# Performance work log

Measured on AMD Instinct MI355X. Metric: run time of the kernel, lower is better.

The kernel has to match this reference:

```python
import jax, jax.numpy as jnp
import numpy as np

EPS = 1e-5

def setup_inputs() -> dict:
    key = jax.random.key(0)
    ks = jax.random.split(key, 8)
    b, c, p, h = 8, 128, 2048, 4
    inp = {
        "input": jax.random.normal(ks[0], (b, c, p), jnp.float32),
        "gamma": jnp.ones((c,), jnp.float32),
        "beta": jnp.zeros((c,), jnp.float32),
        "Wq": jax.random.normal(ks[1], (c * h, c), jnp.float32) * (c ** -0.5),
        "bq": jnp.zeros((c * h,), jnp.float32),
        "Wk": jax.random.normal(ks[2], (c * h, c), jnp.float32) * (c ** -0.5),
        "bk": jnp.zeros((c * h,), jnp.float32),
        "Wv": jax.random.normal(ks[3], (c * h, c), jnp.float32) * (c ** -0.5),
        "bv": jnp.zeros((c * h,), jnp.float32),
        "Wo": jax.random.normal(ks[4], (c, c * h), jnp.float32) * ((c * h) ** -0.5),
        "bo": jnp.zeros((c,), jnp.float32),
    }
    return inp


def reference(input, gamma, beta, Wq, bq, Wk, bk, Wv, bv, Wo, bo):
    b, c, p = input.shape
    h = Wq.shape[0] // c
    # BatchNorm1d (training-mode batch stats): mean/var per channel over (batch, points)
    mean = jnp.mean(input, axis=(0, 2), keepdims=True)          # [1,c,1]
    var = jnp.mean((input - mean) ** 2, axis=(0, 2), keepdims=True)
    x = (input - mean) * jax.lax.rsqrt(var + EPS)
    x = x * gamma[None, :, None] + beta[None, :, None]
    # 1x1 conv projections == channel matmuls; then split c*h -> (c, h)
    q = (jnp.einsum('oc,bcp->bop', Wq, x) + bq[None, :, None]).reshape(b, c, h, p)
    k = (jnp.einsum('oc,bcp->bop', Wk, x) + bk[None, :, None]).reshape(b, c, h, p)
    v = (jnp.einsum('oc,bcp->bop', Wv, x) + bv[None, :, None]).reshape(b, c, h, p)
    # attention over points; scale by c**-0.5
    weight = jnp.einsum('bchi,bchj->bhij', q, k) * (c ** -0.5)   # [b,h,p,p]
    weight = jax.nn.softmax(weight, axis=3)
    att = jnp.einsum('bhij,bchj->bchi', weight, v)               # [b,c,h,p]
    att = att.reshape(b, c * h, p)
    out = jnp.einsum('oc,bcp->bop', Wo, att) + bo[None, :, None]
    return out + input
```

## Files before the change

### kernel.cpp

```cpp
#include <hip/hip_runtime.h>
#include <hip/hip_bf16.h>

#define NB 8
#define NC 128
#define NP 2048
#define NH 4
#define NCH 512

typedef __attribute__((ext_vector_type(8))) short bf16x8;
typedef __attribute__((ext_vector_type(16))) float f32x16;

__device__ __forceinline__ float bf2f(unsigned short u) {
  return __uint_as_float(((unsigned)u) << 16);
}
__device__ __forceinline__ unsigned short f2bf(float f) {
  __hip_bfloat16 h = __float2bfloat16(f);
  return *reinterpret_cast<unsigned short*>(&h);
}
__device__ __forceinline__ unsigned cvtpk(float lo, float hi) {
  unsigned r;
  asm("v_cvt_pk_bf16_f32 %0, %1, %2" : "=v"(r) : "v"(lo), "v"(hi));
  return r;
}
__device__ __forceinline__ void gload_lds16(const void* g, void* l) {
  __builtin_amdgcn_global_load_lds(
      (const __attribute__((address_space(1))) void*)g,
      (__attribute__((address_space(3))) void*)l, 16, 0, 0);
}
__device__ __forceinline__ void plswap(unsigned& a, unsigned& b) {
  asm volatile("v_permlane32_swap_b32 %0, %1" : "+v"(a), "+v"(b));
}

__global__ __launch_bounds__(256) void bn_partial(
    const float* __restrict__ in, float* __restrict__ psum,
    float* __restrict__ psum2) {
  int c = blockIdx.x >> 2, qtr = blockIdx.x & 3;
  int t = threadIdx.x;
  float s = 0.f, s2 = 0.f;
  for (int b = 0; b < NB; ++b) {
    const float* ptr = in + ((size_t)b * NC + c) * NP + qtr * 512;
    #pragma unroll
    for (int p = 0; p < 2; ++p) {
      float v = ptr[p * 256 + t];
      s += v; s2 += v * v;
    }
  }
  for (int off = 32; off; off >>= 1) {
    s += __shfl_down(s, off, 64);
    s2 += __shfl_down(s2, off, 64);
  }
  __shared__ float red[8];
  int lane = t & 63, wid = t >> 6;
  if (!lane) { red[wid] = s; red[wid + 4] = s2; }
  __syncthreads();
  if (!t) {
    psum[blockIdx.x] = red[0] + red[1] + red[2] + red[3];
    psum2[blockIdx.x] = red[4] + red[5] + red[6] + red[7];
  }
}

__global__ __launch_bounds__(512, 2) void qkv_proj(
    const float* __restrict__ in, const float* __restrict__ gamma,
    const float* __restrict__ beta, const float* __restrict__ psum,
    const float* __restrict__ psum2, const float* __restrict__ Wq,
    const float* __restrict__ bq, const float* __restrict__ Wk,
    const float* __restrict__ bk, const float* __restrict__ Wv,
    const float* __restrict__ bv, unsigned short* __restrict__ qws,
    unsigned short* __restrict__ kws, unsigned short* __restrict__ vws) {
  __shared__ float sc[128], sh[128], bias[1536];
  __shared__ __align__(16) unsigned short Xt[64][136];
  int t = threadIdx.x;
  int pt = blockIdx.x & 31, b = blockIdx.x >> 5;
  int p0 = pt * 64;
  if (t < 128) {
    float s = psum[t * 4] + psum[t * 4 + 1] + psum[t * 4 + 2] + psum[t * 4 + 3];
    float s2 = psum2[t * 4] + psum2[t * 4 + 1] + psum2[t * 4 + 2] + psum2[t * 4 + 3];
    const float invn = 1.f / (NB * NP);
    float mean = s * invn, var = s2 * invn - mean * mean;
    float scl = gamma[t] * rsqrtf(var + 1e-5f);
    sc[t] = scl; sh[t] = beta[t] - mean * scl;
  }
  bias[t] = bq[t]; bias[512 + t] = bk[t]; bias[1024 + t] = bv[t];
  __syncthreads();
  {
    int p = t & 63, c0 = (t >> 6) * 16;
    const float* src = in + ((size_t)b * NC + c0) * NP + p0 + p;
    #pragma unroll
    for (int q = 0; q < 8; ++q) {
      float v0 = src[(size_t)(2 * q) * NP] * sc[c0 + 2 * q] + sh[c0 + 2 * q];
      float v1 = src[(size_t)(2 * q + 1) * NP] * sc[c0 + 2 * q + 1] + sh[c0 + 2 * q + 1];
      *(unsigned*)&Xt[p][c0 + 2 * q] = cvtpk(v0, v1);
    }
  }
  __syncthreads();
  int w = t >> 6, lane = t & 63, l31 = lane & 31, h5 = lane >> 5;
  #pragma unroll 1
  for (int s = 0; s < 3; ++s) {
    int strip = s * 8 + w;
    int proj = strip >> 3, sw8 = strip & 7;
    int within = sw8 * 64;
    int hq = sw8 >> 1, cr = (sw8 & 1) * 64;
    const float* W = proj == 0 ? Wq : (proj == 1 ? Wk : Wv);
    int orow[2];
    #pragma unroll
    for (int mt = 0; mt < 2; ++mt)
      orow[mt] = proj < 2 ? (cr + mt * 32 + l31) * 4 + hq
                          : within + mt * 32 + l31;
    f32x16 acc[2][2] = {};
    #pragma unroll
    for (int ks = 0; ks < 8; ++ks) {
      bf16x8 af[2], bf[2];
      #pragma unroll
      for (int mt = 0; mt < 2; ++mt) {
        const float* wr = W + (size_t)orow[mt] * NC + ks * 16 + h5 * 8;
        float4 a = *(const float4*)wr, b4 = *(const float4*)(wr + 4);
        union { bf16x8 v; unsigned u[4]; } uu;
        uu.u[0] = cvtpk(a.x, a.y); uu.u[1] = cvtpk(a.z, a.w);
        uu.u[2] = cvtpk(b4.x, b4.y); uu.u[3] = cvtpk(b4.z, b4.w);
        af[mt] = uu.v;
      }
      #pragma unroll
      for (int nt = 0; nt < 2; ++nt)
        bf[nt] = *(const bf16x8*)&Xt[nt * 32 + l31][ks * 16 + h5 * 8];
      if (proj < 2) {
        #pragma unroll
        for (int mt = 0; mt < 2; ++mt)
          #pragma unroll
          for (int nt = 0; nt < 2; ++nt)
            acc[mt][nt] = __builtin_amdgcn_mfma_f32_32x32x16_bf16(bf[nt], af[mt], acc[mt][nt], 0, 0, 0);
      } else {
        #pragma unroll
        for (int mt = 0; mt < 2; ++mt)
          #pragma unroll
          for (int nt = 0; nt < 2; ++nt)
            acc[mt][nt] = __builtin_amdgcn_mfma_f32_32x32x16_bf16(af[mt], bf[nt], acc[mt][nt], 0, 0, 0);
      }
    }
    if (proj < 2) {
      unsigned short* dst = proj == 0 ? qws : kws;
      float qs = proj == 0 ? 0.12751743762765621f : 1.0f;
      #pragma unroll
      for (int mt = 0; mt < 2; ++mt) {
        int c = cr + mt * 32 + l31;
        int o = c * 4 + hq;
        float bs = bias[proj * 512 + o];
        int g = hq * 128 + c;
        unsigned short* drow = dst + (size_t)b * NP * NCH + g;
        #pragma unroll
        for (int nt = 0; nt < 2; ++nt)
          #pragma unroll
          for (int r2 = 0; r2 < 8; ++r2) {
            int r = r2 * 2;
            unsigned pr = cvtpk((acc[mt][nt][r] + bs) * qs,
                                (acc[mt][nt][r + 1] + bs) * qs);
            int p = p0 + nt * 32 + (r & 3) + 8 * (r >> 2) + 4 * h5;
            drow[(size_t)p * NCH] = (unsigned short)pr;
            drow[(size_t)(p + 1) * NCH] = (unsigned short)(pr >> 16);
          }
      }
    } else {
      #pragma unroll
      for (int mt = 0; mt < 2; ++mt)
        #pragma unroll
        for (int nt = 0; nt < 2; ++nt) {
          int pp = p0 + nt * 32 + l31;
          #pragma unroll
          for (int r2 = 0; r2 < 8; ++r2) {
            int r = r2 * 2;
            int oo = within + mt * 32 + (r & 3) + 8 * (r >> 2) + 4 * h5;
            unsigned pr = cvtpk(acc[mt][nt][r] + bias[1024 + oo],
                                acc[mt][nt][r + 1] + bias[1024 + oo + 1]);
            vws[((size_t)(b * NCH + oo)) * NP + pp] = (unsigned short)pr;
            vws[((size_t)(b * NCH + oo + 1)) * NP + pp] = (unsigned short)(pr >> 16);
          }
        }
    }
  }
}

__global__ __launch_bounds__(256, 2) void attn(
    const unsigned short* __restrict__ qT, const unsigned short* __restrict__ kT,
    const unsigned short* __restrict__ vws, unsigned short* __restrict__ attws) {
  __shared__ uint4 Kbuf[2][1024];
  __shared__ uint4 Vbuf[2][1024];
  int tid = threadIdx.x;
  int wl = tid >> 6, lane = tid & 63, l31 = lane & 31, h5 = lane >> 5;
  int bid = blockIdx.x;
  int b = bid & 7;
  int rest = bid >> 3;
  int hh = rest & 3, it = rest >> 2;
  int i0 = it * 128;
  const unsigned short* kb = kT + (size_t)b * NP * NCH;
  const unsigned short* vb = vws + (size_t)b * NCH * NP;

  int t4 = tid >> 4;
  int ch = (tid & 15) ^ (t4 & 15);
  size_t vO = ((size_t)((t4 * 2 + (ch >> 3)) * 4 + hh)) * NP + (ch & 7) * 8;

  auto stage = [&](int bi, int j0v) {
    #pragma unroll
    for (int k = 0; k < 4; ++k) {
      gload_lds16(kb + (size_t)(j0v + k * 16 + t4) * NCH + hh * 128 + (ch << 3),
                  &Kbuf[bi][k * 256 + tid]);
      gload_lds16(vb + vO + (size_t)k * 128 * NP + j0v,
                  &Vbuf[bi][k * 256 + tid]);
    }
  };

  bf16x8 qf[8];
  {
    const unsigned short* qp =
        qT + ((size_t)b * NP + (i0 + wl * 32 + l31)) * NCH + hh * 128 + h5 * 8;
    #pragma unroll
    for (int ks = 0; ks < 8; ++ks) qf[ks] = *(const bf16x8*)(qp + ks * 16);
  }

  f32x16 oacc[4] = {};
  float lsum = 0.f;

  stage(0, 0);
  __syncthreads();

  int kbase = l31 * 16, ksw = l31 & 15;
  #pragma unroll 1
  for (int tI = 0; tI < 32; ++tI) {
    int cur = tI & 1;
    if (tI < 31) stage(cur ^ 1, (tI + 1) * 64);

    f32x16 sacT0 = {}, sacT1 = {};
    __builtin_amdgcn_s_setprio(1);
    #pragma unroll
    for (int ks = 0; ks < 8; ++ks) {
      int cidx = (ks * 2 + h5) ^ ksw;
      bf16x8 kf0 = *(const bf16x8*)&Kbuf[cur][kbase + cidx];
      bf16x8 kf1 = *(const bf16x8*)&Kbuf[cur][512 + kbase + cidx];
      sacT0 = __builtin_amdgcn_mfma_f32_32x32x16_bf16(kf0, qf[ks], sacT0, 0, 0, 0);
      sacT1 = __builtin_amdgcn_mfma_f32_32x32x16_bf16(kf1, qf[ks], sacT1, 0, 0, 0);
    }
    __builtin_amdgcn_s_setprio(0);
    bf16x8 pfrag[4];
    #pragma unroll
    for (int ntj = 0; ntj < 2; ++ntj) {
      f32x16& sacT = ntj ? sacT1 : sacT0;
      #pragma unroll
      for (int r = 0; r < 16; ++r) {
        sacT[r] = __builtin_amdgcn_exp2f(sacT[r]);
        lsum += sacT[r];
      }
      unsigned wv[8];
      #pragma unroll
      for (int q = 0; q < 8; ++q) wv[q] = cvtpk(sacT[q * 2], sacT[q * 2 + 1]);
      plswap(wv[0], wv[2]); plswap(wv[1], wv[3]);
      plswap(wv[4], wv[6]); plswap(wv[5], wv[7]);
      union { bf16x8 v; unsigned u[4]; } f0, f1;
      f0.u[0] = wv[0]; f0.u[1] = wv[1]; f0.u[2] = wv[2]; f0.u[3] = wv[3];
      f1.u[0] = wv[4]; f1.u[1] = wv[5]; f1.u[2] = wv[6]; f1.u[3] = wv[7];
      pfrag[ntj * 2] = f0.v; pfrag[ntj * 2 + 1] = f1.v;
    }
    __builtin_amdgcn_s_setprio(1);
    #pragma unroll
    for (int ntc = 0; ntc < 4; ++ntc) {
      int r = ntc * 16 + (l31 >> 1);
      int rb = r * 16, r15 = r & 15, c8 = (l31 & 1) * 8;
      #pragma unroll
      for (int kw = 0; kw < 4; ++kw) {
        bf16x8 vf = *(const bf16x8*)&Vbuf[cur][rb + ((c8 + kw * 2 + h5) ^ r15)];
        oacc[ntc] = __builtin_amdgcn_mfma_f32_32x32x16_bf16(vf, pfrag[kw], oacc[ntc], 0, 0, 0);
      }
    }
    __builtin_amdgcn_s_setprio(0);
    __syncthreads();
  }

  float linv = 1.0f / (lsum + __shfl_xor(lsum, 32, 64));
  unsigned short* TB = (unsigned short*)Kbuf;
  int iL = wl * 32 + l31;
  int isw = iL & 7;
  #pragma unroll
  for (int ntc = 0; ntc < 4; ++ntc)
    #pragma unroll
    for (int r2 = 0; r2 < 8; ++r2) {
      int r = r2 * 2;
      int c = ntc * 32 + (r & 3) + 8 * (r >> 2) + 4 * h5;
      unsigned pr = cvtpk(oacc[ntc][r] * linv, oacc[ntc][r + 1] * linv);
      *(unsigned*)&TB[iL * 128 + (((c >> 3) ^ isw) << 3) + (c & 7)] = pr;
    }
  __syncthreads();
  {
    int i2 = tid >> 1, half = tid & 1;
    unsigned short* gp = attws + ((size_t)b * NP + i0 + i2) * NCH + hh * 128 + half * 64;
    const unsigned short* rp = TB + i2 * 128;
    int sw2 = i2 & 7;
    #pragma unroll
    for (int q = 0; q < 8; ++q) {
      int ck = half * 8 + q;
      uint4 v = *(const uint4*)(rp + ((ck ^ sw2) << 3));
      *(uint4*)(gp + q * 8) = v;
    }
  }
}

__global__ __launch_bounds__(256) void wo_perm(
    const float* __restrict__ Wo, unsigned short* __restrict__ WoP) {
  int idx = (blockIdx.x * 256 + threadIdx.x) * 4;
  int o = idx >> 9, g0 = idx & 511;
  int hh = g0 >> 7;
  const float* src = Wo + (size_t)o * NCH + (g0 & 127) * 4 + hh;
  union { unsigned short u[4]; uint2 v; } tmp;
  #pragma unroll
  for (int e = 0; e < 4; ++e) tmp.u[e] = f2bf(src[e * 4]);
  *(uint2*)(WoP + idx) = tmp.v;
}

__global__ __launch_bounds__(256, 2) void out_proj(
    const unsigned short* __restrict__ attT, const unsigned short* __restrict__ WoP,
    const float* __restrict__ bo, const float* __restrict__ in,
    float* __restrict__ out) {
  __shared__ uint4 Abuf[2][512];
  int t = threadIdx.x;
  int pt = blockIdx.x & 63, b = blockIdx.x >> 6;
  int p0 = pt * 32;
  int w = t >> 6, lane = t & 63, l31 = lane & 31, h5 = lane >> 5;
  const unsigned short* ab = attT + (size_t)b * NP * NCH;
  int row0 = t >> 4, pos = t & 15;
  auto stage = [&](int bi, int k0) {
    #pragma unroll
    for (int q = 0; q < 2; ++q) {
      int row = q * 16 + row0;
      int chq = pos ^ (row & 15);
      gload_lds16(ab + ((size_t)(p0 + row)) * NCH + k0 * 128 + chq * 8,
                  &Abuf[bi][q * 256 + t]);
    }
  };
  f32x16 acc = {};
  stage(0, 0);
  __syncthreads();
  #pragma unroll 1
  for (int k0 = 0; k0 < 4; ++k0) {
    int cur = k0 & 1;
    if (k0 < 3) stage(cur ^ 1, k0 + 1);
    #pragma unroll
    for (int ks = 0; ks < 8; ++ks) {
      bf16x8 af = *(const bf16x8*)(WoP + (size_t)(w * 32 + l31) * NCH + k0 * 128 + ks * 16 + h5 * 8);
      bf16x8 bf = *(const bf16x8*)&Abuf[cur][l31 * 16 + ((ks * 2 + h5) ^ (l31 & 15))];
      acc = __builtin_amdgcn_mfma_f32_32x32x16_bf16(af, bf, acc, 0, 0, 0);
    }
    __syncthreads();
  }
  #pragma unroll
  for (int r = 0; r < 16; ++r) {
    int o = w * 32 + (r & 3) + 8 * (r >> 2) + 4 * h5;
    int p = p0 + l31;
    size_t idx = ((size_t)(b * NC + o)) * NP + p;
    out[idx] = acc[r] + bo[o] + in[idx];
  }
}

extern "C" void kernel_launch(void* const* d_in, const int* in_sizes, int n_in,
                              void* d_out, int out_size, void* d_ws, size_t ws_size,
                              hipStream_t stream) {
  const float* in    = (const float*)d_in[0];
  const float* gamma = (const float*)d_in[1];
  const float* beta  = (const float*)d_in[2];
  const float* Wq = (const float*)d_in[3];
  const float* bq = (const float*)d_in[4];
  const float* Wk = (const float*)d_in[5];
  const float* bk = (const float*)d_in[6];
  const float* Wv = (const float*)d_in[7];
  const float* bv = (const float*)d_in[8];
  const float* Wo = (const float*)d_in[9];
  const float* bo = (const float*)d_in[10];
  float* out = (float*)d_out;

  char* ws = (char*)d_ws;
  float* psum  = (float*)ws;
  float* psum2 = psum + 512;
  const size_t QKV_ELEMS = (size_t)NB * NCH * NP;
  unsigned short* qws   = (unsigned short*)(ws + 8192);
  unsigned short* kws   = qws + QKV_ELEMS;
  unsigned short* vws   = kws + QKV_ELEMS;
  unsigned short* attws = vws + QKV_ELEMS;
  unsigned short* WoP   = qws;

  bn_partial<<<dim3(512), dim3(256), 0, stream>>>(in, psum, psum2);
  qkv_proj<<<dim3(256), dim3(512), 0, stream>>>(
      in, gamma, beta, psum, psum2, Wq, bq, Wk, bk, Wv, bv, qws, kws, vws);
  attn<<<dim3(512), dim3(256), 0, stream>>>(qws, kws, vws, attws);
  wo_perm<<<dim3(64), dim3(256), 0, stream>>>(Wo, WoP);
  out_proj<<<dim3(512), dim3(256), 0, stream>>>(attws, WoP, bo, in, out);
}
```

Measured before the change: 198.7 us.

## Pre-convert weights to bf16 in BN kernel and interleave softmax with PV MFMAs

Weight fp32-to-bf16 conversion for Wq/Wk/Wv and the Wo permutation are folded into the bn_partial kernel. This removes the separate wo_perm launch and the per-block redundant weight conversion inside qkv_proj, at the cost of extra workspace and more work in bn_partial. In the attention loop, the exp/pack of the second score tile is now placed between the two halves of the P·V MFMAs, so VALU exp work can overlap matrix work. The permlane swap asm is also made non-volatile to give the scheduler freedom.

```diff
diff --git a/kernel.cpp b/kernel.cpp
--- a/kernel.cpp
+++ b/kernel.cpp
@@ -28,14 +28,33 @@
       (__attribute__((address_space(3))) void*)l, 16, 0, 0);
 }
 __device__ __forceinline__ void plswap(unsigned& a, unsigned& b) {
-  asm volatile("v_permlane32_swap_b32 %0, %1" : "+v"(a), "+v"(b));
+  asm("v_permlane32_swap_b32 %0, %1" : "+v"(a), "+v"(b));
 }
 
 __global__ __launch_bounds__(256) void bn_partial(
     const float* __restrict__ in, float* __restrict__ psum,
-    float* __restrict__ psum2) {
+    float* __restrict__ psum2,
+    const float* __restrict__ Wq, const float* __restrict__ Wk,
+    const float* __restrict__ Wv, const float* __restrict__ Wo,
+    unsigned short* __restrict__ wqb, unsigned short* __restrict__ wkb,
+    unsigned short* __restrict__ wvb, unsigned short* __restrict__ wop) {
   int c = blockIdx.x >> 2, qtr = blockIdx.x & 3;
   int t = threadIdx.x;
+  {
+    int gt = blockIdx.x * 256 + t;
+    int m = gt >> 15, i = gt & 32767;
+    if (m < 3) {
+      const float* src = m == 0 ? Wq : (m == 1 ? Wk : Wv);
+      unsigned short* dst = m == 0 ? wqb : (m == 1 ? wkb : wvb);
+      *(unsigned*)(dst + i * 2) = cvtpk(src[i * 2], src[i * 2 + 1]);
+    } else {
+      int e0 = i * 2;
+      int o = e0 >> 9, g0 = e0 & 511;
+      int hh = g0 >> 7, cc = g0 & 127;
+      const float* srow = Wo + (size_t)o * NCH + hh;
+      *(unsigned*)(wop + e0) = cvtpk(srow[cc * 4], srow[(cc + 1) * 4]);
+    }
+  }
   float s = 0.f, s2 = 0.f;
   for (int b = 0; b < NB; ++b) {
     const float* ptr = in + ((size_t)b * NC + c) * NP + qtr * 512;
@@ -62,9 +81,9 @@
 __global__ __launch_bounds__(512, 2) void qkv_proj(
     const float* __restrict__ in, const float* __restrict__ gamma,
     const float* __restrict__ beta, const float* __restrict__ psum,
-    const float* __restrict__ psum2, const float* __restrict__ Wq,
-    const float* __restrict__ bq, const float* __restrict__ Wk,
-    const float* __restrict__ bk, const float* __restrict__ Wv,
+    const float* __restrict__ psum2, const unsigned short* __restrict__ wqb,
+    const float* __restrict__ bq, const unsigned short* __restrict__ wkb,
+    const float* __restrict__ bk, const unsigned short* __restrict__ wvb,
     const float* __restrict__ bv, unsigned short* __restrict__ qws,
     unsigned short* __restrict__ kws, unsigned short* __restrict__ vws) {
   __shared__ float sc[128], sh[128], bias[1536];
@@ -100,7 +119,7 @@
     int proj = strip >> 3, sw8 = strip & 7;
     int within = sw8 * 64;
     int hq = sw8 >> 1, cr = (sw8 & 1) * 64;
-    const float* W = proj == 0 ? Wq : (proj == 1 ? Wk : Wv);
+    const unsigned short* WB = proj == 0 ? wqb : (proj == 1 ? wkb : wvb);
     int orow[2];
     #pragma unroll
     for (int mt = 0; mt < 2; ++mt)
@@ -111,14 +130,8 @@
     for (int ks = 0; ks < 8; ++ks) {
       bf16x8 af[2], bf[2];
       #pragma unroll
-      for (int mt = 0; mt < 2; ++mt) {
-        const float* wr = W + (size_t)orow[mt] * NC + ks * 16 + h5 * 8;
-        float4 a = *(const float4*)wr, b4 = *(const float4*)(wr + 4);
-        union { bf16x8 v; unsigned u[4]; } uu;
-        uu.u[0] = cvtpk(a.x, a.y); uu.u[1] = cvtpk(a.z, a.w);
-        uu.u[2] = cvtpk(b4.x, b4.y); uu.u[3] = cvtpk(b4.z, b4.w);
-        af[mt] = uu.v;
-      }
+      for (int mt = 0; mt < 2; ++mt)
+        af[mt] = *(const bf16x8*)(WB + (size_t)orow[mt] * NC + ks * 16 + h5 * 8);
       #pragma unroll
       for (int nt = 0; nt < 2; ++nt)
         bf[nt] = *(const bf16x8*)&Xt[nt * 32 + l31][ks * 16 + h5 * 8];
@@ -238,35 +251,58 @@
       sacT1 = __builtin_amdgcn_mfma_f32_32x32x16_bf16(kf1, qf[ks], sacT1, 0, 0, 0);
     }
     __builtin_amdgcn_s_setprio(0);
-    bf16x8 pfrag[4];
-    #pragma unroll
-    for (int ntj = 0; ntj < 2; ++ntj) {
-      f32x16& sacT = ntj ? sacT1 : sacT0;
+
+    bf16x8 pfA0, pfA1, pfB0, pfB1;
+    {
       #pragma unroll
       for (int r = 0; r < 16; ++r) {
-        sacT[r] = __builtin_amdgcn_exp2f(sacT[r]);
-        lsum += sacT[r];
+        sacT0[r] = __builtin_amdgcn_exp2f(sacT0[r]);
+        lsum += sacT0[r];
       }
       unsigned wv[8];
       #pragma unroll
-      for (int q = 0; q < 8; ++q) wv[q] = cvtpk(sacT[q * 2], sacT[q * 2 + 1]);
+      for (int q = 0; q < 8; ++q) wv[q] = cvtpk(sacT0[q * 2], sacT0[q * 2 + 1]);
       plswap(wv[0], wv[2]); plswap(wv[1], wv[3]);
       plswap(wv[4], wv[6]); plswap(wv[5], wv[7]);
       union { bf16x8 v; unsigned u[4]; } f0, f1;
       f0.u[0] = wv[0]; f0.u[1] = wv[1]; f0.u[2] = wv[2]; f0.u[3] = wv[3];
       f1.u[0] = wv[4]; f1.u[1] = wv[5]; f1.u[2] = wv[6]; f1.u[3] = wv[7];
-      pfrag[ntj * 2] = f0.v; pfrag[ntj * 2 + 1] = f1.v;
-    }
-    __builtin_amdgcn_s_setprio(1);
+      pfA0 = f0.v; pfA1 = f1.v;
+    }
     #pragma unroll
     for (int ntc = 0; ntc < 4; ++ntc) {
       int r = ntc * 16 + (l31 >> 1);
       int rb = r * 16, r15 = r & 15, c8 = (l31 & 1) * 8;
-      #pragma unroll
-      for (int kw = 0; kw < 4; ++kw) {
-        bf16x8 vf = *(const bf16x8*)&Vbuf[cur][rb + ((c8 + kw * 2 + h5) ^ r15)];
-        oacc[ntc] = __builtin_amdgcn_mfma_f32_32x32x16_bf16(vf, pfrag[kw], oacc[ntc], 0, 0, 0);
+      bf16x8 vf0 = *(const bf16x8*)&Vbuf[cur][rb + ((c8 + 0 + h5) ^ r15)];
+      bf16x8 vf1 = *(const bf16x8*)&Vbuf[cur][rb + ((c8 + 2 + h5) ^ r15)];
+      oacc[ntc] = __builtin_amdgcn_mfma_f32_32x32x16_bf16(vf0, pfA0, oacc[ntc], 0, 0, 0);
+      oacc[ntc] = __builtin_amdgcn_mfma_f32_32x32x16_bf16(vf1, pfA1, oacc[ntc], 0, 0, 0);
+    }
+    {
+      #pragma unroll
+      for (int r = 0; r < 16; ++r) {
+        sacT1[r] = __builtin_amdgcn_exp2f(sacT1[r]);
+        lsum += sacT1[r];
       }
+      unsigned wv[8];
+      #pragma unroll
+      for (int q = 0; q < 8; ++q) wv[q] = cvtpk(sacT1[q * 2], sacT1[q * 2 + 1]);
+      plswap(wv[0], wv[2]); plswap(wv[1], wv[3]);
+      plswap(wv[4], wv[6]); plswap(wv[5], wv[7]);
+      union { bf16x8 v; unsigned u[4]; } f0, f1;
+      f0.u[0] = wv[0]; f0.u[1] = wv[1]; f0.u[2] = wv[2]; f0.u[3] = wv[3];
+      f1.u[0] = wv[4]; f1.u[1] = wv[5]; f1.u[2] = wv[6]; f1.u[3] = wv[7];
+      pfB0 = f0.v; pfB1 = f1.v;
+    }
+    __builtin_amdgcn_s_setprio(1);
+    #pragma unroll
+    for (int ntc = 0; ntc < 4; ++ntc) {
+      int r = ntc * 16 + (l31 >> 1);
+      int rb = r * 16, r15 = r & 15, c8 = (l31 & 1) * 8;
+      bf16x8 vf2 = *(const bf16x8*)&Vbuf[cur][rb + ((c8 + 4 + h5) ^ r15)];
+      bf16x8 vf3 = *(const bf16x8*)&Vbuf[cur][rb + ((c8 + 6 + h5) ^ r15)];
+      oacc[ntc] = __builtin_amdgcn_mfma_f32_32x32x16_bf16(vf2, pfB0, oacc[ntc], 0, 0, 0);
+      oacc[ntc] = __builtin_amdgcn_mfma_f32_32x32x16_bf16(vf3, pfB1, oacc[ntc], 0, 0, 0);
     }
     __builtin_amdgcn_s_setprio(0);
     __syncthreads();
@@ -298,18 +334,6 @@
       *(uint4*)(gp + q * 8) = v;
     }
   }
-}
-
-__global__ __launch_bounds__(256) void wo_perm(
-    const float* __restrict__ Wo, unsigned short* __restrict__ WoP) {
-  int idx = (blockIdx.x * 256 + threadIdx.x) * 4;
-  int o = idx >> 9, g0 = idx & 511;
-  int hh = g0 >> 7;
-  const float* src = Wo + (size_t)o * NCH + (g0 & 127) * 4 + hh;
-  union { unsigned short u[4]; uint2 v; } tmp;
-  #pragma unroll
-  for (int e = 0; e < 4; ++e) tmp.u[e] = f2bf(src[e * 4]);
-  *(uint2*)(WoP + idx) = tmp.v;
 }
 
 __global__ __launch_bounds__(256, 2) void out_proj(
@@ -375,17 +399,20 @@
   char* ws = (char*)d_ws;
   float* psum  = (float*)ws;
   float* psum2 = psum + 512;
+  unsigned short* wqb = (unsigned short*)(ws + 8192);
+  unsigned short* wkb = wqb + 65536;
+  unsigned short* wvb = wkb + 65536;
+  unsigned short* wop = wvb + 65536;
   const size_t QKV_ELEMS = (size_t)NB * NCH * NP;
-  unsigned short* qws   = (unsigned short*)(ws + 8192);
+  unsigned short* qws   = wop + 65536;
   unsigned short* kws   = qws + QKV_ELEMS;
   unsigned short* vws   = kws + QKV_ELEMS;
   unsigned short* attws = vws + QKV_ELEMS;
-  unsigned short* WoP   = qws;
-
-  bn_partial<<<dim3(512), dim3(256), 0, stream>>>(in, psum, psum2);
+
+  bn_partial<<<dim3(512), dim3(256), 0, stream>>>(
+      in, psum, psum2, Wq, Wk, Wv, Wo, wqb, wkb, wvb, wop);
   qkv_proj<<<dim3(256), dim3(512), 0, stream>>>(
-      in, gamma, beta, psum, psum2, Wq, bq, Wk, bk, Wv, bv, qws, kws, vws);
+      in, gamma, beta, psum, psum2, wqb, bq, wkb, bk, wvb, bv, qws, kws, vws);
   attn<<<dim3(512), dim3(256), 0, stream>>>(qws, kws, vws, attws);
-  wo_perm<<<dim3(64), dim3(256), 0, stream>>>(Wo, WoP);
-  out_proj<<<dim3(512), dim3(256), 0, stream>>>(attws, WoP, bo, in, out);
-}
+  out_proj<<<dim3(512), dim3(256), 0, stream>>>(attws, wop, bo, in, out);
+}
```

Measured after the change: 185.6 us. -6.6%, faster.
